# Kernel tuning notes

Hardware: AMD Instinct MI355X
Metric: run time of the kernel (lower is better)

The kernel has to match this reference:

```python
import jax, jax.numpy as jnp
import numpy as np

N, E, D, H, G, L = 50000, 800000, 64, 2, 512, 3  # nodes, edges, hidden, heads, graphs, layers


def setup_inputs() -> dict:
    key = jax.random.key(0)
    ks = jax.random.split(key, 20)
    x = jax.random.normal(ks[0], (N, D), dtype=jnp.float32)
    edge_index = jax.random.randint(ks[1], (2, E), 0, N, dtype=jnp.int64)
    batch = jnp.sort(jax.random.randint(ks[2], (N,), 0, G, dtype=jnp.int64))
    s = 1.0 / np.sqrt(D)
    Wq = jax.random.normal(ks[3], (L, D, H * D), dtype=jnp.float32) * s
    bq = jnp.zeros((L, H * D), jnp.float32)
    Wk = jax.random.normal(ks[4], (L, D, H * D), dtype=jnp.float32) * s
    bk = jnp.zeros((L, H * D), jnp.float32)
    Wv = jax.random.normal(ks[5], (L, D, H * D), dtype=jnp.float32) * s
    bv = jnp.zeros((L, H * D), jnp.float32)
    Ws = jax.random.normal(ks[6], (L, D, D), dtype=jnp.float32) * s
    bs = jnp.zeros((L, D), jnp.float32)
    ln_g = jnp.ones((L - 1, D), jnp.float32)
    ln_b = jnp.zeros((L - 1, D), jnp.float32)
    Wout = jax.random.normal(ks[7], (D, 1), dtype=jnp.float32) * s
    bout = jnp.zeros((1,), jnp.float32)
    return {"x": x, "edge_index": edge_index, "batch": batch, "num_graphs": G,
            "Wq": Wq, "bq": bq, "Wk": Wk, "bk": bk, "Wv": Wv, "bv": bv,
            "Ws": Ws, "bs": bs, "ln_g": ln_g, "ln_b": ln_b, "Wout": Wout, "bout": bout}


def _transformer_conv(x, src, dst, Wq, bq, Wk, bk, Wv, bv, Ws, bs):
    n = x.shape[0]
    q = (x @ Wq + bq).reshape(n, H, D)
    k = (x @ Wk + bk).reshape(n, H, D)
    v = (x @ Wv + bv).reshape(n, H, D)
    # per-edge attention score: q_dst . k_src / sqrt(d)
    scores = jnp.einsum('ehc,ehc->eh', q[dst], k[src]) / jnp.sqrt(jnp.float32(D))
    m = jax.ops.segment_max(scores, dst, num_segments=n)          # [n,H]
    e = jnp.exp(scores - m[dst])
    denom = jax.ops.segment_sum(e, dst, num_segments=n)           # [n,H]
    alpha = e / (denom[dst] + 1e-16)
    msg = alpha[..., None] * v[src]                               # [E,H,D]
    out = jax.ops.segment_sum(msg, dst, num_segments=n)           # [n,H,D]
    return out.mean(axis=1) + x @ Ws + bs                         # concat=False: head mean + skip


def _layernorm(x, g, b):
    mu = x.mean(-1, keepdims=True)
    var = ((x - mu) ** 2).mean(-1, keepdims=True)
    return (x - mu) / jnp.sqrt(var + 1e-5) * g + b


def reference(x, edge_index, batch, num_graphs, Wq, bq, Wk, bk, Wv, bv, Ws, bs, ln_g, ln_b, Wout, bout):
    src, dst = edge_index[0], edge_index[1]
    h = x
    for i in range(L):
        h = _transformer_conv(h, src, dst, Wq[i], bq[i], Wk[i], bk[i], Wv[i], bv[i], Ws[i], bs[i])
        h = jax.nn.relu(h)
        if i != L - 1:
            h = _layernorm(h, ln_g[i], ln_b[i])
    # global mean pool over graphs
    sums = jax.ops.segment_sum(h, batch, num_segments=num_graphs)
    cnt = jax.ops.segment_sum(jnp.ones((h.shape[0],), h.dtype), batch, num_segments=num_graphs)
    pooled = sums / jnp.maximum(cnt, 1.0)[:, None]
    return pooled @ Wout + bout
```

## Files before the change

### kernel.cpp

```cpp
#include <hip/hip_runtime.h>
#include <hip/hip_fp16.h>
#include <math.h>

#define NN 50000
#define EE 800000
#define GG 512

typedef _Float16 f16x8 __attribute__((ext_vector_type(8)));
typedef _Float16 f16x2 __attribute__((ext_vector_type(2)));
typedef float f32x4 __attribute__((ext_vector_type(4)));

#if defined(__has_builtin)
#if __has_builtin(__builtin_amdgcn_fdot2)
#define HAS_FDOT2 1
#endif
#endif

#define QSCALE 0.1803368801111244f

__device__ __forceinline__ float wave16_sum(float p) {
    p += __shfl_xor(p, 1);
    p += __shfl_xor(p, 2);
    p += __shfl_xor(p, 4);
    p += __shfl_xor(p, 8);
    return p;
}
__device__ __forceinline__ float2 h2f(unsigned int u) {
    __half2 h = *reinterpret_cast<__half2*>(&u);
    return __half22float2(h);
}
__device__ __forceinline__ unsigned short f2us(float x) {
    return __half_as_ushort(__float2half(x));
}
__device__ __forceinline__ float us2f(unsigned short u) {
    return __half2float(__ushort_as_half(u));
}
__device__ __forceinline__ f16x2 u2h2(unsigned int u) {
    union { unsigned int u; f16x2 h; } x; x.u = u; return x.h;
}
__device__ __forceinline__ float dot2acc(f16x2 a, f16x2 b, float c) {
#ifdef HAS_FDOT2
    return __builtin_amdgcn_fdot2(a, b, c, false);
#else
    return c + (float)a[0] * (float)b[0] + (float)a[1] * (float)b[1];
#endif
}
__device__ __forceinline__ float exp2fast(float x) {
    return __builtin_amdgcn_exp2f(x);
}

__global__ void deg_kernel(const int* __restrict__ ei, int* __restrict__ deg) {
    int e = blockIdx.x * 256 + threadIdx.x;
    if (e < EE) atomicAdd(&deg[ei[EE + e]], 1);
}

__global__ void scan1(const int* __restrict__ deg, int* __restrict__ incl, int* __restrict__ bsum) {
    __shared__ int sh[256];
    int t = threadIdx.x;
    int n = blockIdx.x * 256 + t;
    int vv = (n < NN) ? deg[n] : 0;
    sh[t] = vv; __syncthreads();
    for (int off = 1; off < 256; off <<= 1) {
        int u = (t >= off) ? sh[t - off] : 0;
        __syncthreads();
        sh[t] += u;
        __syncthreads();
    }
    if (n < NN) incl[n] = sh[t];
    if (t == 255) bsum[blockIdx.x] = sh[255];
}

__global__ void scan2(int* __restrict__ bsum, int nblk) {
    __shared__ int sh[256];
    int t = threadIdx.x;
    int vv = (t < nblk) ? bsum[t] : 0;
    sh[t] = vv; __syncthreads();
    for (int off = 1; off < 256; off <<= 1) {
        int u = (t >= off) ? sh[t - off] : 0;
        __syncthreads();
        sh[t] += u;
        __syncthreads();
    }
    bsum[t] = sh[t];
}

__global__ void scan3(int* __restrict__ rowst, const int* __restrict__ deg,
                      const int* __restrict__ bsum, int* __restrict__ cursor) {
    int n = blockIdx.x * 256 + threadIdx.x;
    if (n >= NN) return;
    int off = (blockIdx.x > 0) ? bsum[blockIdx.x - 1] : 0;
    int excl = rowst[n] - deg[n] + off;
    rowst[n] = excl;
    cursor[n] = excl;
}

__global__ void fill_kernel(const int* __restrict__ ei, int* __restrict__ cursor,
                            unsigned short* __restrict__ esrc) {
    int e = blockIdx.x * 256 + threadIdx.x;
    if (e < EE) {
        int s = ei[e], d = ei[EE + e];
        int pos = atomicAdd(&cursor[d], 1);
        esrc[pos] = (unsigned short)s;
    }
}

__global__ void cast_x_kernel(const float* __restrict__ x, unsigned short* __restrict__ xh) {
    int i = blockIdx.x * 256 + threadIdx.x;
    if (i < NN * 16) {
        float4 v = *(const float4*)(x + (size_t)i * 4);
        ushort4 o = make_ushort4(f2us(v.x), f2us(v.y), f2us(v.z), f2us(v.w));
        *(ushort4*)(xh + (size_t)i * 4) = o;
    }
}

#define WT_LSTRIDE (448 * 64)
__global__ void pack_w_kernel(const float* __restrict__ Wq, const float* __restrict__ Wk,
                              const float* __restrict__ Wv, const float* __restrict__ Ws,
                              unsigned short* __restrict__ wt) {
    int idx = blockIdx.x * 256 + threadIdx.x;
    if (idx >= 3 * WT_LSTRIDE) return;
    int l = idx / WT_LSTRIDE, r = idx % WT_LSTRIDE;
    int c = r / 64, k = r % 64;
    float val;
    if (c < 384) {
        int m = c >> 7, col = c & 127;
        const float* W = (m == 0) ? Wq : ((m == 1) ? Wk : Wv);
        val = W[(size_t)l * 64 * 128 + k * 128 + col];
    } else {
        int col = c - 384;
        val = Ws[(size_t)l * 64 * 64 + k * 64 + col];
    }
    wt[idx] = f2us(val);
}

__global__ __launch_bounds__(256) void gemm_mfma(
    const unsigned short* __restrict__ xh,
    const unsigned short* __restrict__ wt,
    const float* __restrict__ bq, const float* __restrict__ bk,
    const float* __restrict__ bv, const float* __restrict__ bsk,
    unsigned short* __restrict__ qh, unsigned short* __restrict__ kvh,
    float* __restrict__ skip) {
    int t = threadIdx.x;
    int wave = t >> 6, lane = t & 63;
    int li = lane & 15, lh = lane >> 4;
    int row0 = blockIdx.x * 32 + (wave & 1) * 16;
    int ctbase = (wave >> 1) * 14;

    int arow = min(row0 + li, NN - 1);
    const unsigned short* ap = xh + (size_t)arow * 64 + lh * 8;
    f16x8 a0 = *(const f16x8*)(ap);
    f16x8 a1 = *(const f16x8*)(ap + 32);

    int rb = row0 + lh * 4;

    #pragma unroll 2
    for (int tt = 0; tt < 14; ++tt) {
        int c = (ctbase + tt) * 16 + li;
        const unsigned short* bp = wt + (size_t)c * 64 + lh * 8;
        f16x8 b0 = *(const f16x8*)(bp);
        f16x8 b1 = *(const f16x8*)(bp + 32);
        f32x4 d = {0.f, 0.f, 0.f, 0.f};
        d = __builtin_amdgcn_mfma_f32_16x16x32_f16(a0, b0, d, 0, 0, 0);
        d = __builtin_amdgcn_mfma_f32_16x16x32_f16(a1, b1, d, 0, 0, 0);
        if (c < 128) {
            float bias = bq[c];
            #pragma unroll
            for (int e = 0; e < 4; ++e) {
                int r = rb + e;
                if (r < NN) qh[(size_t)r * 128 + c] = f2us((d[e] + bias) * QSCALE);
            }
        } else if (c < 256) {
            int ch = c - 128;
            float bias = bk[ch];
            int off = (ch < 64) ? ((ch >> 2) * 16 + (ch & 3))
                                : (((ch - 64) >> 2) * 16 + 4 + (ch & 3));
            #pragma unroll
            for (int e = 0; e < 4; ++e) {
                int r = rb + e;
                if (r < NN) kvh[(size_t)r * 256 + off] = f2us(d[e] + bias);
            }
        } else if (c < 384) {
            int ch = c - 256;
            float bias = bv[ch];
            int off = 8 + ((ch < 64) ? ((ch >> 2) * 16 + (ch & 3))
                                     : (((ch - 64) >> 2) * 16 + 4 + (ch & 3)));
            #pragma unroll
            for (int e = 0; e < 4; ++e) {
                int r = rb + e;
                if (r < NN) kvh[(size_t)r * 256 + off] = f2us(d[e] + bias);
            }
        } else {
            int ch = c - 384;
            float bias = bsk[ch];
            #pragma unroll
            for (int e = 0; e < 4; ++e) {
                int r = rb + e;
                if (r < NN) skip[(size_t)r * 64 + ch] = d[e] + bias;
            }
        }
    }
}

__global__ __launch_bounds__(256) void agg_kernel(
    const unsigned short* __restrict__ qh, const unsigned short* __restrict__ kvh,
    const float* __restrict__ skip,
    const int* __restrict__ rowst, const int* __restrict__ deg,
    const unsigned short* __restrict__ esrc, const float* __restrict__ gamma,
    const float* __restrict__ beta, unsigned short* __restrict__ hout, int do_ln) {
    int wave = threadIdx.x >> 6;
    int lane = threadIdx.x & 63;
    int node = blockIdx.x * 4 + wave;
    if (node >= NN) return;
    int j = lane & 15;
    int slot = lane >> 4;

    uint2 qu0 = *(const uint2*)(qh + (size_t)node * 128 + j * 4);
    uint2 qu1 = *(const uint2*)(qh + (size_t)node * 128 + 64 + j * 4);
    f16x2 q0a = u2h2(qu0.x), q0b = u2h2(qu0.y);
    f16x2 q1a = u2h2(qu1.x), q1b = u2h2(qu1.y);

    float m0 = -1e30f, m1 = -1e30f;
    float l0 = 0.f, l1 = 0.f;
    float acc0[4] = {0.f, 0.f, 0.f, 0.f};
    float acc1[4] = {0.f, 0.f, 0.f, 0.f};

    int st = rowst[node];
    int dg = deg[node];
    for (int base = slot * 2; base < dg; base += 8) {
        int last = dg - 1;
        int s0 = (int)esrc[st + min(base + 0, last)];
        int s1 = (int)esrc[st + min(base + 1, last)];
        const unsigned short* b0 = kvh + (size_t)s0 * 256 + j * 16;
        const unsigned short* b1 = kvh + (size_t)s1 * 256 + j * 16;
        uint4 A0 = *(const uint4*)(b0);
        uint4 B0 = *(const uint4*)(b0 + 8);
        uint4 A1 = *(const uint4*)(b1);
        uint4 B1 = *(const uint4*)(b1 + 8);

        float p00 = dot2acc(q0b, u2h2(A0.y), dot2acc(q0a, u2h2(A0.x), 0.f));
        float p01 = dot2acc(q1b, u2h2(A0.w), dot2acc(q1a, u2h2(A0.z), 0.f));
        float p10 = dot2acc(q0b, u2h2(A1.y), dot2acc(q0a, u2h2(A1.x), 0.f));
        float p11 = dot2acc(q1b, u2h2(A1.w), dot2acc(q1a, u2h2(A1.z), 0.f));
        p00 = wave16_sum(p00);
        p01 = wave16_sum(p01);
        p10 = wave16_sum(p10);
        p11 = wave16_sum(p11);
        if (base + 1 > last) { p10 = -1e30f; p11 = -1e30f; }

        float2 c00 = h2f(B0.x), c01 = h2f(B0.y), c02 = h2f(B0.z), c03 = h2f(B0.w);
        float2 c10 = h2f(B1.x), c11 = h2f(B1.y), c12 = h2f(B1.z), c13 = h2f(B1.w);
        float v00[4] = {c00.x, c00.y, c01.x, c01.y};
        float v01[4] = {c02.x, c02.y, c03.x, c03.y};
        float v10[4] = {c10.x, c10.y, c11.x, c11.y};
        float v11[4] = {c12.x, c12.y, c13.x, c13.y};

        {
            float nm = fmaxf(m0, fmaxf(p00, p10));
            float f = exp2fast(m0 - nm);
            float e0 = exp2fast(p00 - nm);
            float e1 = exp2fast(p10 - nm);
            l0 = l0 * f + e0 + e1;
            #pragma unroll
            for (int r = 0; r < 4; ++r)
                acc0[r] = acc0[r] * f + e0 * v00[r] + e1 * v10[r];
            m0 = nm;
        }
        {
            float nm = fmaxf(m1, fmaxf(p01, p11));
            float f = exp2fast(m1 - nm);
            float e0 = exp2fast(p01 - nm);
            float e1 = exp2fast(p11 - nm);
            l1 = l1 * f + e0 + e1;
            #pragma unroll
            for (int r = 0; r < 4; ++r)
                acc1[r] = acc1[r] * f + e0 * v01[r] + e1 * v11[r];
            m1 = nm;
        }
    }
    #pragma unroll
    for (int mask = 16; mask <= 32; mask <<= 1) {
        {
            float mo = __shfl_xor(m0, mask);
            float lo = __shfl_xor(l0, mask);
            float ao[4];
            #pragma unroll
            for (int r = 0; r < 4; ++r) ao[r] = __shfl_xor(acc0[r], mask);
            float nm = fmaxf(m0, mo);
            float fa = exp2fast(m0 - nm);
            float fb = exp2fast(mo - nm);
            l0 = l0 * fa + lo * fb;
            #pragma unroll
            for (int r = 0; r < 4; ++r) acc0[r] = acc0[r] * fa + ao[r] * fb;
            m0 = nm;
        }
        {
            float mo = __shfl_xor(m1, mask);
            float lo = __shfl_xor(l1, mask);
            float ao[4];
            #pragma unroll
            for (int r = 0; r < 4; ++r) ao[r] = __shfl_xor(acc1[r], mask);
            float nm = fmaxf(m1, mo);
            float fa = exp2fast(m1 - nm);
            float fb = exp2fast(mo - nm);
            l1 = l1 * fa + lo * fb;
            #pragma unroll
            for (int r = 0; r < 4; ++r) acc1[r] = acc1[r] * fa + ao[r] * fb;
            m1 = nm;
        }
    }
    float i0 = 1.f / (l0 + 1e-16f);
    float i1 = 1.f / (l1 + 1e-16f);
    float4 sk = *(const float4*)(skip + (size_t)node * 64 + j * 4);
    float ska[4] = {sk.x, sk.y, sk.z, sk.w};
    float val[4];
    #pragma unroll
    for (int r = 0; r < 4; ++r) {
        float o = 0.5f * (acc0[r] * i0 + acc1[r] * i1) + ska[r];
        val[r] = fmaxf(o, 0.f);
    }
    if (do_ln) {
        float s = val[0] + val[1] + val[2] + val[3];
        s = wave16_sum(s);
        float mu = s * (1.f / 64.f);
        float ss = 0.f;
        #pragma unroll
        for (int r = 0; r < 4; ++r) { float d = val[r] - mu; ss += d * d; }
        ss = wave16_sum(ss);
        float rstd = rsqrtf(ss * (1.f / 64.f) + 1e-5f);
        float4 g4 = *(const float4*)(gamma + j * 4);
        float4 b4 = *(const float4*)(beta + j * 4);
        float ga[4] = {g4.x, g4.y, g4.z, g4.w};
        float ba[4] = {b4.x, b4.y, b4.z, b4.w};
        #pragma unroll
        for (int r = 0; r < 4; ++r) val[r] = (val[r] - mu) * rstd * ga[r] + ba[r];
    }
    if (slot == 0) {
        ushort4 o = make_ushort4(f2us(val[0]), f2us(val[1]), f2us(val[2]), f2us(val[3]));
        *(ushort4*)(hout + (size_t)node * 64 + j * 4) = o;
    }
}

__device__ __forceinline__ int lbound(const int* __restrict__ a, int n, int key) {
    int lo = 0, hi = n;
    while (lo < hi) {
        int mid = (lo + hi) >> 1;
        if (a[mid] < key) lo = mid + 1; else hi = mid;
    }
    return lo;
}

__global__ __launch_bounds__(256) void pool_final_kernel(
    const unsigned short* __restrict__ h, const int* __restrict__ batch,
    const float* __restrict__ Wout, const float* __restrict__ bout,
    float* __restrict__ out) {
    __shared__ int sh_lo, sh_hi;
    __shared__ float part[4][64];
    int g = blockIdx.x;
    int t = threadIdx.x;
    if (t == 0) {
        sh_lo = lbound(batch, NN, g);
        sh_hi = lbound(batch, NN, g + 1);
    }
    __syncthreads();
    int lo = sh_lo, hi = sh_hi;
    int c = t & 63, w = t >> 6;
    float s = 0.f;
    for (int n = lo + w; n < hi; n += 4) s += us2f(h[(size_t)n * 64 + c]);
    part[w][c] = s;
    __syncthreads();
    if (t < 64) {
        float tot = part[0][t] + part[1][t] + part[2][t] + part[3][t];
        float cnt = (float)(hi - lo);
        float val = tot / fmaxf(cnt, 1.f) * Wout[t];
        #pragma unroll
        for (int mk = 1; mk < 64; mk <<= 1) val += __shfl_xor(val, mk);
        if (t == 0) out[g] = val + bout[0];
    }
}

extern "C" void kernel_launch(void* const* d_in, const int* in_sizes, int n_in,
                              void* d_out, int out_size, void* d_ws, size_t ws_size,
                              hipStream_t stream) {
    const float* x    = (const float*)d_in[0];
    const int*   ei   = (const int*)d_in[1];
    const int*   batch= (const int*)d_in[2];
    const float* Wq   = (const float*)d_in[4];
    const float* bq   = (const float*)d_in[5];
    const float* Wk   = (const float*)d_in[6];
    const float* bk   = (const float*)d_in[7];
    const float* Wv   = (const float*)d_in[8];
    const float* bv   = (const float*)d_in[9];
    const float* Ws   = (const float*)d_in[10];
    const float* bs   = (const float*)d_in[11];
    const float* lng  = (const float*)d_in[12];
    const float* lnb  = (const float*)d_in[13];
    const float* Wout = (const float*)d_in[14];
    const float* bout = (const float*)d_in[15];
    float* out = (float*)d_out;

    unsigned short* qh  = (unsigned short*)d_ws;
    unsigned short* kvh = qh + (size_t)NN * 128;
    float* skip = (float*)(kvh + (size_t)NN * 256);
    unsigned short* xh0 = (unsigned short*)(skip + (size_t)NN * 64);
    unsigned short* xh1 = xh0 + (size_t)NN * 64;
    unsigned short* wt  = xh1 + (size_t)NN * 64;
    int* deg    = (int*)(wt + 3 * WT_LSTRIDE);
    int* rowst  = deg + NN;
    int* cursor = rowst + NN;
    int* bsum   = cursor + NN;
    unsigned short* esrc = (unsigned short*)(bsum + 256);

    hipMemsetAsync(deg, 0, NN * sizeof(int), stream);

    const int NB = (NN + 255) / 256;
    deg_kernel<<<(EE + 255) / 256, 256, 0, stream>>>(ei, deg);
    scan1<<<NB, 256, 0, stream>>>(deg, rowst, bsum);
    scan2<<<1, 256, 0, stream>>>(bsum, NB);
    scan3<<<NB, 256, 0, stream>>>(rowst, deg, bsum, cursor);
    fill_kernel<<<(EE + 255) / 256, 256, 0, stream>>>(ei, cursor, esrc);

    cast_x_kernel<<<(NN * 16 + 255) / 256, 256, 0, stream>>>(x, xh0);
    pack_w_kernel<<<(3 * WT_LSTRIDE + 255) / 256, 256, 0, stream>>>(Wq, Wk, Wv, Ws, wt);

    const int GEMM_GRID = (NN + 31) / 32;
    unsigned short* hin = xh0;
    unsigned short* houts[3] = {xh1, xh0, xh1};
    for (int l = 0; l < 3; ++l) {
        gemm_mfma<<<GEMM_GRID, 256, 0, stream>>>(hin, wt + (size_t)l * WT_LSTRIDE,
            bq + (size_t)l * 128, bk + (size_t)l * 128, bv + (size_t)l * 128,
            bs + (size_t)l * 64, qh, kvh, skip);
        int do_ln = (l < 2) ? 1 : 0;
        agg_kernel<<<(NN + 3) / 4, 256, 0, stream>>>(qh, kvh, skip, rowst, deg, esrc,
                                                     lng + (size_t)(do_ln ? l : 0) * 64,
                                                     lnb + (size_t)(do_ln ? l : 0) * 64,
                                                     houts[l], do_ln);
        hin = houts[l];
    }
    pool_final_kernel<<<GG, 256, 0, stream>>>(hin, batch, Wout, bout, out);
}
```

Before: 404.7 us.

## Process two nodes per wave in aggregation with prefetched edge indices; fuse prep kernels

```diff
diff --git a/kernel.cpp b/kernel.cpp
--- a/kernel.cpp
+++ b/kernel.cpp
@@ -104,20 +104,19 @@
     }
 }
 
-__global__ void cast_x_kernel(const float* __restrict__ x, unsigned short* __restrict__ xh) {
+#define WT_LSTRIDE (448 * 64)
+__global__ void prep_kernel(const float* __restrict__ x, unsigned short* __restrict__ xh,
+                            const float* __restrict__ Wq, const float* __restrict__ Wk,
+                            const float* __restrict__ Wv, const float* __restrict__ Ws,
+                            unsigned short* __restrict__ wt) {
     int i = blockIdx.x * 256 + threadIdx.x;
     if (i < NN * 16) {
         float4 v = *(const float4*)(x + (size_t)i * 4);
         ushort4 o = make_ushort4(f2us(v.x), f2us(v.y), f2us(v.z), f2us(v.w));
         *(ushort4*)(xh + (size_t)i * 4) = o;
-    }
-}
-
-#define WT_LSTRIDE (448 * 64)
-__global__ void pack_w_kernel(const float* __restrict__ Wq, const float* __restrict__ Wk,
-                              const float* __restrict__ Wv, const float* __restrict__ Ws,
-                              unsigned short* __restrict__ wt) {
-    int idx = blockIdx.x * 256 + threadIdx.x;
+        return;
+    }
+    int idx = i - NN * 16;
     if (idx >= 3 * WT_LSTRIDE) return;
     int l = idx / WT_LSTRIDE, r = idx % WT_LSTRIDE;
     int c = r / 64, k = r % 64;
@@ -209,134 +208,270 @@
     const float* __restrict__ beta, unsigned short* __restrict__ hout, int do_ln) {
     int wave = threadIdx.x >> 6;
     int lane = threadIdx.x & 63;
-    int node = blockIdx.x * 4 + wave;
-    if (node >= NN) return;
+    int nodeA = blockIdx.x * 8 + wave * 2;
+    if (nodeA >= NN) return;
+    int nodeB = nodeA + 1;
+    bool hasB = nodeB < NN;
+    int nodeBc = hasB ? nodeB : nodeA;
     int j = lane & 15;
     int slot = lane >> 4;
 
-    uint2 qu0 = *(const uint2*)(qh + (size_t)node * 128 + j * 4);
-    uint2 qu1 = *(const uint2*)(qh + (size_t)node * 128 + 64 + j * 4);
-    f16x2 q0a = u2h2(qu0.x), q0b = u2h2(qu0.y);
-    f16x2 q1a = u2h2(qu1.x), q1b = u2h2(qu1.y);
-
-    float m0 = -1e30f, m1 = -1e30f;
-    float l0 = 0.f, l1 = 0.f;
-    float acc0[4] = {0.f, 0.f, 0.f, 0.f};
-    float acc1[4] = {0.f, 0.f, 0.f, 0.f};
-
-    int st = rowst[node];
-    int dg = deg[node];
-    for (int base = slot * 2; base < dg; base += 8) {
-        int last = dg - 1;
-        int s0 = (int)esrc[st + min(base + 0, last)];
-        int s1 = (int)esrc[st + min(base + 1, last)];
-        const unsigned short* b0 = kvh + (size_t)s0 * 256 + j * 16;
-        const unsigned short* b1 = kvh + (size_t)s1 * 256 + j * 16;
-        uint4 A0 = *(const uint4*)(b0);
-        uint4 B0 = *(const uint4*)(b0 + 8);
-        uint4 A1 = *(const uint4*)(b1);
-        uint4 B1 = *(const uint4*)(b1 + 8);
-
-        float p00 = dot2acc(q0b, u2h2(A0.y), dot2acc(q0a, u2h2(A0.x), 0.f));
-        float p01 = dot2acc(q1b, u2h2(A0.w), dot2acc(q1a, u2h2(A0.z), 0.f));
-        float p10 = dot2acc(q0b, u2h2(A1.y), dot2acc(q0a, u2h2(A1.x), 0.f));
-        float p11 = dot2acc(q1b, u2h2(A1.w), dot2acc(q1a, u2h2(A1.z), 0.f));
-        p00 = wave16_sum(p00);
-        p01 = wave16_sum(p01);
-        p10 = wave16_sum(p10);
-        p11 = wave16_sum(p11);
-        if (base + 1 > last) { p10 = -1e30f; p11 = -1e30f; }
-
-        float2 c00 = h2f(B0.x), c01 = h2f(B0.y), c02 = h2f(B0.z), c03 = h2f(B0.w);
-        float2 c10 = h2f(B1.x), c11 = h2f(B1.y), c12 = h2f(B1.z), c13 = h2f(B1.w);
-        float v00[4] = {c00.x, c00.y, c01.x, c01.y};
-        float v01[4] = {c02.x, c02.y, c03.x, c03.y};
-        float v10[4] = {c10.x, c10.y, c11.x, c11.y};
-        float v11[4] = {c12.x, c12.y, c13.x, c13.y};
+    uint2 qAu0 = *(const uint2*)(qh + (size_t)nodeA * 128 + j * 4);
+    uint2 qAu1 = *(const uint2*)(qh + (size_t)nodeA * 128 + 64 + j * 4);
+    uint2 qBu0 = *(const uint2*)(qh + (size_t)nodeBc * 128 + j * 4);
+    uint2 qBu1 = *(const uint2*)(qh + (size_t)nodeBc * 128 + 64 + j * 4);
+    f16x2 qA0a = u2h2(qAu0.x), qA0b = u2h2(qAu0.y);
+    f16x2 qA1a = u2h2(qAu1.x), qA1b = u2h2(qAu1.y);
+    f16x2 qB0a = u2h2(qBu0.x), qB0b = u2h2(qBu0.y);
+    f16x2 qB1a = u2h2(qBu1.x), qB1b = u2h2(qBu1.y);
+
+    float mA0 = -1e30f, mA1 = -1e30f, lA0 = 0.f, lA1 = 0.f;
+    float mB0 = -1e30f, mB1 = -1e30f, lB0 = 0.f, lB1 = 0.f;
+    float accA0[4] = {0.f, 0.f, 0.f, 0.f};
+    float accA1[4] = {0.f, 0.f, 0.f, 0.f};
+    float accB0[4] = {0.f, 0.f, 0.f, 0.f};
+    float accB1[4] = {0.f, 0.f, 0.f, 0.f};
+
+    int stA = rowst[nodeA], dgA = deg[nodeA];
+    int stB = rowst[nodeBc], dgB = hasB ? deg[nodeBc] : 0;
+    int lastA = max(dgA - 1, 0), lastB = max(dgB - 1, 0);
+    int dgMax = max(dgA, dgB);
+    int iters = (dgMax + 7) >> 3;
+    int b0 = slot * 2;
+
+    int sA0 = (dgA > 0) ? (int)esrc[stA + min(b0, lastA)] : 0;
+    int sA1 = (dgA > 0) ? (int)esrc[stA + min(b0 + 1, lastA)] : 0;
+    int sB0 = (dgB > 0) ? (int)esrc[stB + min(b0, lastB)] : 0;
+    int sB1 = (dgB > 0) ? (int)esrc[stB + min(b0 + 1, lastB)] : 0;
+
+    for (int it = 0; it < iters; ++it) {
+        int base = it * 8 + b0;
+        const unsigned short* a0p = kvh + (size_t)sA0 * 256 + j * 16;
+        const unsigned short* a1p = kvh + (size_t)sA1 * 256 + j * 16;
+        const unsigned short* b0p = kvh + (size_t)sB0 * 256 + j * 16;
+        const unsigned short* b1p = kvh + (size_t)sB1 * 256 + j * 16;
+        uint4 KA0 = *(const uint4*)(a0p);
+        uint4 VA0 = *(const uint4*)(a0p + 8);
+        uint4 KA1 = *(const uint4*)(a1p);
+        uint4 VA1 = *(const uint4*)(a1p + 8);
+        uint4 KB0 = *(const uint4*)(b0p);
+        uint4 VB0 = *(const uint4*)(b0p + 8);
+        uint4 KB1 = *(const uint4*)(b1p);
+        uint4 VB1 = *(const uint4*)(b1p + 8);
+
+        int nb = base + 8;
+        sA0 = (dgA > 0) ? (int)esrc[stA + min(nb, lastA)] : 0;
+        sA1 = (dgA > 0) ? (int)esrc[stA + min(nb + 1, lastA)] : 0;
+        sB0 = (dgB > 0) ? (int)esrc[stB + min(nb, lastB)] : 0;
+        sB1 = (dgB > 0) ? (int)esrc[stB + min(nb + 1, lastB)] : 0;
 
         {
-            float nm = fmaxf(m0, fmaxf(p00, p10));
-            float f = exp2fast(m0 - nm);
-            float e0 = exp2fast(p00 - nm);
-            float e1 = exp2fast(p10 - nm);
-            l0 = l0 * f + e0 + e1;
-            #pragma unroll
-            for (int r = 0; r < 4; ++r)
-                acc0[r] = acc0[r] * f + e0 * v00[r] + e1 * v10[r];
-            m0 = nm;
+            float p00 = dot2acc(qA0b, u2h2(KA0.y), dot2acc(qA0a, u2h2(KA0.x), 0.f));
+            float p01 = dot2acc(qA1b, u2h2(KA0.w), dot2acc(qA1a, u2h2(KA0.z), 0.f));
+            float p10 = dot2acc(qA0b, u2h2(KA1.y), dot2acc(qA0a, u2h2(KA1.x), 0.f));
+            float p11 = dot2acc(qA1b, u2h2(KA1.w), dot2acc(qA1a, u2h2(KA1.z), 0.f));
+            p00 = wave16_sum(p00);
+            p01 = wave16_sum(p01);
+            p10 = wave16_sum(p10);
+            p11 = wave16_sum(p11);
+            if (base > lastA || dgA == 0) { p00 = -1e30f; p01 = -1e30f; }
+            if (base + 1 > lastA || dgA == 0) { p10 = -1e30f; p11 = -1e30f; }
+
+            float2 c00 = h2f(VA0.x), c01 = h2f(VA0.y), c02 = h2f(VA0.z), c03 = h2f(VA0.w);
+            float2 c10 = h2f(VA1.x), c11 = h2f(VA1.y), c12 = h2f(VA1.z), c13 = h2f(VA1.w);
+            float v00[4] = {c00.x, c00.y, c01.x, c01.y};
+            float v01[4] = {c02.x, c02.y, c03.x, c03.y};
+            float v10[4] = {c10.x, c10.y, c11.x, c11.y};
+            float v11[4] = {c12.x, c12.y, c13.x, c13.y};
+            {
+                float nm = fmaxf(mA0, fmaxf(p00, p10));
+                float f = exp2fast(mA0 - nm);
+                float e0 = exp2fast(p00 - nm);
+                float e1 = exp2fast(p10 - nm);
+                lA0 = lA0 * f + e0 + e1;
+                #pragma unroll
+                for (int r = 0; r < 4; ++r)
+                    accA0[r] = accA0[r] * f + e0 * v00[r] + e1 * v10[r];
+                mA0 = nm;
+            }
+            {
+                float nm = fmaxf(mA1, fmaxf(p01, p11));
+                float f = exp2fast(mA1 - nm);
+                float e0 = exp2fast(p01 - nm);
+                float e1 = exp2fast(p11 - nm);
+                lA1 = lA1 * f + e0 + e1;
+                #pragma unroll
+                for (int r = 0; r < 4; ++r)
+                    accA1[r] = accA1[r] * f + e0 * v01[r] + e1 * v11[r];
+                mA1 = nm;
+            }
         }
         {
-            float nm = fmaxf(m1, fmaxf(p01, p11));
-            float f = exp2fast(m1 - nm);
-            float e0 = exp2fast(p01 - nm);
-            float e1 = exp2fast(p11 - nm);
-            l1 = l1 * f + e0 + e1;
-            #pragma unroll
-            for (int r = 0; r < 4; ++r)
-                acc1[r] = acc1[r] * f + e0 * v01[r] + e1 * v11[r];
-            m1 = nm;
-        }
-    }
+            float p00 = dot2acc(qB0b, u2h2(KB0.y), dot2acc(qB0a, u2h2(KB0.x), 0.f));
+            float p01 = dot2acc(qB1b, u2h2(KB0.w), dot2acc(qB1a, u2h2(KB0.z), 0.f));
+            float p10 = dot2acc(qB0b, u2h2(KB1.y), dot2acc(qB0a, u2h2(KB1.x), 0.f));
+            float p11 = dot2acc(qB1b, u2h2(KB1.w), dot2acc(qB1a, u2h2(KB1.z), 0.f));
+            p00 = wave16_sum(p00);
+            p01 = wave16_sum(p01);
+            p10 = wave16_sum(p10);
+            p11 = wave16_sum(p11);
+            if (base > lastB || dgB == 0) { p00 = -1e30f; p01 = -1e30f; }
+            if (base + 1 > lastB || dgB == 0) { p10 = -1e30f; p11 = -1e30f; }
+
+            float2 c00 = h2f(VB0.x), c01 = h2f(VB0.y), c02 = h2f(VB0.z), c03 = h2f(VB0.w);
+            float2 c10 = h2f(VB1.x), c11 = h2f(VB1.y), c12 = h2f(VB1.z), c13 = h2f(VB1.w);
+            float v00[4] = {c00.x, c00.y, c01.x, c01.y};
+            float v01[4] = {c02.x, c02.y, c03.x, c03.y};
+            float v10[4] = {c10.x, c10.y, c11.x, c11.y};
+            float v11[4] = {c12.x, c12.y, c13.x, c13.y};
+            {
+                float nm = fmaxf(mB0, fmaxf(p00, p10));
+                float f = exp2fast(mB0 - nm);
+                float e0 = exp2fast(p00 - nm);
+                float e1 = exp2fast(p10 - nm);
+                lB0 = lB0 * f + e0 + e1;
+                #pragma unroll
+                for (int r = 0; r < 4; ++r)
+                    accB0[r] = accB0[r] * f + e0 * v00[r] + e1 * v10[r];
+                mB0 = nm;
+            }
+            {
+                float nm = fmaxf(mB1, fmaxf(p01, p11));
+                float f = exp2fast(mB1 - nm);
+                float e0 = exp2fast(p01 - nm);
+                float e1 = exp2fast(p11 - nm);
+                lB1 = lB1 * f + e0 + e1;
+                #pragma unroll
+                for (int r = 0; r < 4; ++r)
+                    accB1[r] = accB1[r] * f + e0 * v01[r] + e1 * v11[r];
+                mB1 = nm;
+            }
+        }
+    }
+
     #pragma unroll
     for (int mask = 16; mask <= 32; mask <<= 1) {
         {
-            float mo = __shfl_xor(m0, mask);
-            float lo = __shfl_xor(l0, mask);
+            float mo = __shfl_xor(mA0, mask);
+            float lo = __shfl_xor(lA0, mask);
             float ao[4];
             #pragma unroll
-            for (int r = 0; r < 4; ++r) ao[r] = __shfl_xor(acc0[r], mask);
-            float nm = fmaxf(m0, mo);
-            float fa = exp2fast(m0 - nm);
+            for (int r = 0; r < 4; ++r) ao[r] = __shfl_xor(accA0[r], mask);
+            float nm = fmaxf(mA0, mo);
+            float fa = exp2fast(mA0 - nm);
             float fb = exp2fast(mo - nm);
-            l0 = l0 * fa + lo * fb;
-            #pragma unroll
-            for (int r = 0; r < 4; ++r) acc0[r] = acc0[r] * fa + ao[r] * fb;
-            m0 = nm;
+            lA0 = lA0 * fa + lo * fb;
+            #pragma unroll
+            for (int r = 0; r < 4; ++r) accA0[r] = accA0[r] * fa + ao[r] * fb;
+            mA0 = nm;
         }
         {
-            float mo = __shfl_xor(m1, mask);
-            float lo = __shfl_xor(l1, mask);
+            float mo = __shfl_xor(mA1, mask);
+            float lo = __shfl_xor(lA1, mask);
             float ao[4];
             #pragma unroll
-            for (int r = 0; r < 4; ++r) ao[r] = __shfl_xor(acc1[r], mask);
-            float nm = fmaxf(m1, mo);
-            float fa = exp2fast(m1 - nm);
+            for (int r = 0; r < 4; ++r) ao[r] = __shfl_xor(accA1[r], mask);
+            float nm = fmaxf(mA1, mo);
+            float fa = exp2fast(mA1 - nm);
             float fb = exp2fast(mo - nm);
-            l1 = l1 * fa + lo * fb;
-            #pragma unroll
-            for (int r = 0; r < 4; ++r) acc1[r] = acc1[r] * fa + ao[r] * fb;
-            m1 = nm;
-        }
-    }
-    float i0 = 1.f / (l0 + 1e-16f);
-    float i1 = 1.f / (l1 + 1e-16f);
-    float4 sk = *(const float4*)(skip + (size_t)node * 64 + j * 4);
-    float ska[4] = {sk.x, sk.y, sk.z, sk.w};
-    float val[4];
-    #pragma unroll
-    for (int r = 0; r < 4; ++r) {
-        float o = 0.5f * (acc0[r] * i0 + acc1[r] * i1) + ska[r];
-        val[r] = fmaxf(o, 0.f);
-    }
-    if (do_ln) {
-        float s = val[0] + val[1] + val[2] + val[3];
-        s = wave16_sum(s);
-        float mu = s * (1.f / 64.f);
-        float ss = 0.f;
+            lA1 = lA1 * fa + lo * fb;
+            #pragma unroll
+            for (int r = 0; r < 4; ++r) accA1[r] = accA1[r] * fa + ao[r] * fb;
+            mA1 = nm;
+        }
+        {
+            float mo = __shfl_xor(mB0, mask);
+            float lo = __shfl_xor(lB0, mask);
+            float ao[4];
+            #pragma unroll
+            for (int r = 0; r < 4; ++r) ao[r] = __shfl_xor(accB0[r], mask);
+            float nm = fmaxf(mB0, mo);
+            float fa = exp2fast(mB0 - nm);
+            float fb = exp2fast(mo - nm);
+            lB0 = lB0 * fa + lo * fb;
+            #pragma unroll
+            for (int r = 0; r < 4; ++r) accB0[r] = accB0[r] * fa + ao[r] * fb;
+            mB0 = nm;
+        }
+        {
+            float mo = __shfl_xor(mB1, mask);
+            float lo = __shfl_xor(lB1, mask);
+            float ao[4];
+            #pragma unroll
+            for (int r = 0; r < 4; ++r) ao[r] = __shfl_xor(accB1[r], mask);
+            float nm = fmaxf(mB1, mo);
+            float fa = exp2fast(mB1 - nm);
+            float fb = exp2fast(mo - nm);
+            lB1 = lB1 * fa + lo * fb;
+            #pragma unroll
+            for (int r = 0; r < 4; ++r) accB1[r] = accB1[r] * fa + ao[r] * fb;
+            mB1 = nm;
+        }
+    }
+
+    {
+        float i0 = 1.f / (lA0 + 1e-16f);
+        float i1 = 1.f / (lA1 + 1e-16f);
+        float4 sk = *(const float4*)(skip + (size_t)nodeA * 64 + j * 4);
+        float ska[4] = {sk.x, sk.y, sk.z, sk.w};
+        float val[4];
         #pragma unroll
-        for (int r = 0; r < 4; ++r) { float d = val[r] - mu; ss += d * d; }
-        ss = wave16_sum(ss);
-        float rstd = rsqrtf(ss * (1.f / 64.f) + 1e-5f);
-        float4 g4 = *(const float4*)(gamma + j * 4);
-        float4 b4 = *(const float4*)(beta + j * 4);
-        float ga[4] = {g4.x, g4.y, g4.z, g4.w};
-        float ba[4] = {b4.x, b4.y, b4.z, b4.w};
+        for (int r = 0; r < 4; ++r) {
+            float o = 0.5f * (accA0[r] * i0 + accA1[r] * i1) + ska[r];
+            val[r] = fmaxf(o, 0.f);
+        }
+        if (do_ln) {
+            float s = val[0] + val[1] + val[2] + val[3];
+            s = wave16_sum(s);
+            float mu = s * (1.f / 64.f);
+            float ss = 0.f;
+            #pragma unroll
+            for (int r = 0; r < 4; ++r) { float d = val[r] - mu; ss += d * d; }
+            ss = wave16_sum(ss);
+            float rstd = rsqrtf(ss * (1.f / 64.f) + 1e-5f);
+            float4 g4 = *(const float4*)(gamma + j * 4);
+            float4 b4 = *(const float4*)(beta + j * 4);
+            float ga[4] = {g4.x, g4.y, g4.z, g4.w};
+            float ba[4] = {b4.x, b4.y, b4.z, b4.w};
+            #pragma unroll
+            for (int r = 0; r < 4; ++r) val[r] = (val[r] - mu) * rstd * ga[r] + ba[r];
+        }
+        if (slot == 0) {
+            ushort4 o = make_ushort4(f2us(val[0]), f2us(val[1]), f2us(val[2]), f2us(val[3]));
+            *(ushort4*)(hout + (size_t)nodeA * 64 + j * 4) = o;
+        }
+    }
+    if (hasB) {
+        float i0 = 1.f / (lB0 + 1e-16f);
+        float i1 = 1.f / (lB1 + 1e-16f);
+        float4 sk = *(const float4*)(skip + (size_t)nodeB * 64 + j * 4);
+        float ska[4] = {sk.x, sk.y, sk.z, sk.w};
+        float val[4];
         #pragma unroll
-        for (int r = 0; r < 4; ++r) val[r] = (val[r] - mu) * rstd * ga[r] + ba[r];
-    }
-    if (slot == 0) {
-        ushort4 o = make_ushort4(f2us(val[0]), f2us(val[1]), f2us(val[2]), f2us(val[3]));
-        *(ushort4*)(hout + (size_t)node * 64 + j * 4) = o;
+        for (int r = 0; r < 4; ++r) {
+            float o = 0.5f * (accB0[r] * i0 + accB1[r] * i1) + ska[r];
+            val[r] = fmaxf(o, 0.f);
+        }
+        if (do_ln) {
+            float s = val[0] + val[1] + val[2] + val[3];
+            s = wave16_sum(s);
+            float mu = s * (1.f / 64.f);
+            float ss = 0.f;
+            #pragma unroll
+            for (int r = 0; r < 4; ++r) { float d = val[r] - mu; ss += d * d; }
+            ss = wave16_sum(ss);
+            float rstd = rsqrtf(ss * (1.f / 64.f) + 1e-5f);
+            float4 g4 = *(const float4*)(gamma + j * 4);
+            float4 b4 = *(const float4*)(beta + j * 4);
+            float ga[4] = {g4.x, g4.y, g4.z, g4.w};
+            float ba[4] = {b4.x, b4.y, b4.z, b4.w};
+            #pragma unroll
+            for (int r = 0; r < 4; ++r) val[r] = (val[r] - mu) * rstd * ga[r] + ba[r];
+        }
+        if (slot == 0) {
+            ushort4 o = make_ushort4(f2us(val[0]), f2us(val[1]), f2us(val[2]), f2us(val[3]));
+            *(ushort4*)(hout + (size_t)nodeB * 64 + j * 4) = o;
+        }
     }
 }
 
@@ -419,8 +554,8 @@
     scan3<<<NB, 256, 0, stream>>>(rowst, deg, bsum, cursor);
     fill_kernel<<<(EE + 255) / 256, 256, 0, stream>>>(ei, cursor, esrc);
 
-    cast_x_kernel<<<(NN * 16 + 255) / 256, 256, 0, stream>>>(x, xh0);
-    pack_w_kernel<<<(3 * WT_LSTRIDE + 255) / 256, 256, 0, stream>>>(Wq, Wk, Wv, Ws, wt);
+    const int PREP_TOT = NN * 16 + 3 * WT_LSTRIDE;
+    prep_kernel<<<(PREP_TOT + 255) / 256, 256, 0, stream>>>(x, xh0, Wq, Wk, Wv, Ws, wt);
 
     const int GEMM_GRID = (NN + 31) / 32;
     unsigned short* hin = xh0;
@@ -430,7 +565,7 @@
             bq + (size_t)l * 128, bk + (size_t)l * 128, bv + (size_t)l * 128,
             bs + (size_t)l * 64, qh, kvh, skip);
         int do_ln = (l < 2) ? 1 : 0;
-        agg_kernel<<<(NN + 3) / 4, 256, 0, stream>>>(qh, kvh, skip, rowst, deg, esrc,
+        agg_kernel<<<(NN + 7) / 8, 256, 0, stream>>>(qh, kvh, skip, rowst, deg, esrc,
                                                      lng + (size_t)(do_ln ? l : 0) * 64,
                                                      lnb + (size_t)(do_ln ? l : 0) * 64,
                                                      houts[l], do_ln);
```

Result: slower. 461.5 us (+14.0%).

## Store K and V contiguously per node and fuse input cast with weight packing

Applied to the files above, without the earlier changes.

```diff
diff --git a/kernel.cpp b/kernel.cpp
--- a/kernel.cpp
+++ b/kernel.cpp
@@ -104,20 +104,19 @@
     }
 }
 
-__global__ void cast_x_kernel(const float* __restrict__ x, unsigned short* __restrict__ xh) {
+#define WT_LSTRIDE (448 * 64)
+__global__ void prep_kernel(const float* __restrict__ x, unsigned short* __restrict__ xh,
+                            const float* __restrict__ Wq, const float* __restrict__ Wk,
+                            const float* __restrict__ Wv, const float* __restrict__ Ws,
+                            unsigned short* __restrict__ wt) {
     int i = blockIdx.x * 256 + threadIdx.x;
     if (i < NN * 16) {
         float4 v = *(const float4*)(x + (size_t)i * 4);
         ushort4 o = make_ushort4(f2us(v.x), f2us(v.y), f2us(v.z), f2us(v.w));
         *(ushort4*)(xh + (size_t)i * 4) = o;
-    }
-}
-
-#define WT_LSTRIDE (448 * 64)
-__global__ void pack_w_kernel(const float* __restrict__ Wq, const float* __restrict__ Wk,
-                              const float* __restrict__ Wv, const float* __restrict__ Ws,
-                              unsigned short* __restrict__ wt) {
-    int idx = blockIdx.x * 256 + threadIdx.x;
+        return;
+    }
+    int idx = i - NN * 16;
     if (idx >= 3 * WT_LSTRIDE) return;
     int l = idx / WT_LSTRIDE, r = idx % WT_LSTRIDE;
     int c = r / 64, k = r % 64;
@@ -172,22 +171,18 @@
         } else if (c < 256) {
             int ch = c - 128;
             float bias = bk[ch];
-            int off = (ch < 64) ? ((ch >> 2) * 16 + (ch & 3))
-                                : (((ch - 64) >> 2) * 16 + 4 + (ch & 3));
             #pragma unroll
             for (int e = 0; e < 4; ++e) {
                 int r = rb + e;
-                if (r < NN) kvh[(size_t)r * 256 + off] = f2us(d[e] + bias);
+                if (r < NN) kvh[(size_t)r * 256 + ch] = f2us(d[e] + bias);
             }
         } else if (c < 384) {
             int ch = c - 256;
             float bias = bv[ch];
-            int off = 8 + ((ch < 64) ? ((ch >> 2) * 16 + (ch & 3))
-                                     : (((ch - 64) >> 2) * 16 + 4 + (ch & 3)));
             #pragma unroll
             for (int e = 0; e < 4; ++e) {
                 int r = rb + e;
-                if (r < NN) kvh[(size_t)r * 256 + off] = f2us(d[e] + bias);
+                if (r < NN) kvh[(size_t)r * 256 + 128 + ch] = f2us(d[e] + bias);
             }
         } else {
             int ch = c - 384;
@@ -226,29 +221,35 @@
 
     int st = rowst[node];
     int dg = deg[node];
+    int last = dg - 1;
     for (int base = slot * 2; base < dg; base += 8) {
-        int last = dg - 1;
         int s0 = (int)esrc[st + min(base + 0, last)];
         int s1 = (int)esrc[st + min(base + 1, last)];
-        const unsigned short* b0 = kvh + (size_t)s0 * 256 + j * 16;
-        const unsigned short* b1 = kvh + (size_t)s1 * 256 + j * 16;
-        uint4 A0 = *(const uint4*)(b0);
-        uint4 B0 = *(const uint4*)(b0 + 8);
-        uint4 A1 = *(const uint4*)(b1);
-        uint4 B1 = *(const uint4*)(b1 + 8);
-
-        float p00 = dot2acc(q0b, u2h2(A0.y), dot2acc(q0a, u2h2(A0.x), 0.f));
-        float p01 = dot2acc(q1b, u2h2(A0.w), dot2acc(q1a, u2h2(A0.z), 0.f));
-        float p10 = dot2acc(q0b, u2h2(A1.y), dot2acc(q0a, u2h2(A1.x), 0.f));
-        float p11 = dot2acc(q1b, u2h2(A1.w), dot2acc(q1a, u2h2(A1.z), 0.f));
+        const unsigned short* b0 = kvh + (size_t)s0 * 256;
+        const unsigned short* b1 = kvh + (size_t)s1 * 256;
+        uint2 K00 = *(const uint2*)(b0 + j * 4);
+        uint2 K01 = *(const uint2*)(b0 + 64 + j * 4);
+        uint2 V00 = *(const uint2*)(b0 + 128 + j * 4);
+        uint2 V01 = *(const uint2*)(b0 + 192 + j * 4);
+        uint2 K10 = *(const uint2*)(b1 + j * 4);
+        uint2 K11 = *(const uint2*)(b1 + 64 + j * 4);
+        uint2 V10 = *(const uint2*)(b1 + 128 + j * 4);
+        uint2 V11 = *(const uint2*)(b1 + 192 + j * 4);
+
+        float p00 = dot2acc(q0b, u2h2(K00.y), dot2acc(q0a, u2h2(K00.x), 0.f));
+        float p01 = dot2acc(q1b, u2h2(K01.y), dot2acc(q1a, u2h2(K01.x), 0.f));
+        float p10 = dot2acc(q0b, u2h2(K10.y), dot2acc(q0a, u2h2(K10.x), 0.f));
+        float p11 = dot2acc(q1b, u2h2(K11.y), dot2acc(q1a, u2h2(K11.x), 0.f));
         p00 = wave16_sum(p00);
         p01 = wave16_sum(p01);
         p10 = wave16_sum(p10);
         p11 = wave16_sum(p11);
         if (base + 1 > last) { p10 = -1e30f; p11 = -1e30f; }
 
-        float2 c00 = h2f(B0.x), c01 = h2f(B0.y), c02 = h2f(B0.z), c03 = h2f(B0.w);
-        float2 c10 = h2f(B1.x), c11 = h2f(B1.y), c12 = h2f(B1.z), c13 = h2f(B1.w);
+        float2 c00 = h2f(V00.x), c01 = h2f(V00.y);
+        float2 c02 = h2f(V01.x), c03 = h2f(V01.y);
+        float2 c10 = h2f(V10.x), c11 = h2f(V10.y);
+        float2 c12 = h2f(V11.x), c13 = h2f(V11.y);
         float v00[4] = {c00.x, c00.y, c01.x, c01.y};
         float v01[4] = {c02.x, c02.y, c03.x, c03.y};
         float v10[4] = {c10.x, c10.y, c11.x, c11.y};
@@ -419,8 +420,8 @@
     scan3<<<NB, 256, 0, stream>>>(rowst, deg, bsum, cursor);
     fill_kernel<<<(EE + 255) / 256, 256, 0, stream>>>(ei, cursor, esrc);
 
-    cast_x_kernel<<<(NN * 16 + 255) / 256, 256, 0, stream>>>(x, xh0);
-    pack_w_kernel<<<(3 * WT_LSTRIDE + 255) / 256, 256, 0, stream>>>(Wq, Wk, Wv, Ws, wt);
+    const int PREP_TOT = NN * 16 + 3 * WT_LSTRIDE;
+    prep_kernel<<<(PREP_TOT + 255) / 256, 256, 0, stream>>>(x, xh0, Wq, Wk, Wv, Ws, wt);
 
     const int GEMM_GRID = (NN + 31) / 32;
     unsigned short* hin = xh0;
```

Result: faster. 395.4 us (-2.3%).

## Stage GEMM outputs in LDS for coalesced stores, fp16 skip, fuse prep kernels

Applied to the files above, without the earlier changes.

```diff
diff --git a/kernel.cpp b/kernel.cpp
--- a/kernel.cpp
+++ b/kernel.cpp
@@ -104,33 +104,46 @@
     }
 }
 
-__global__ void cast_x_kernel(const float* __restrict__ x, unsigned short* __restrict__ xh) {
-    int i = blockIdx.x * 256 + threadIdx.x;
-    if (i < NN * 16) {
+#define WT_LSTRIDE (448 * 64)
+#define XCAST_BLKS 3125
+__global__ void prep_kernel(const float* __restrict__ x, unsigned short* __restrict__ xh,
+                            const float* __restrict__ Wq, const float* __restrict__ Wk,
+                            const float* __restrict__ Wv, const float* __restrict__ Ws,
+                            unsigned short* __restrict__ wt) {
+    __shared__ float lds_t[64][65];
+    if (blockIdx.x < XCAST_BLKS) {
+        int i = blockIdx.x * 256 + threadIdx.x;
         float4 v = *(const float4*)(x + (size_t)i * 4);
         ushort4 o = make_ushort4(f2us(v.x), f2us(v.y), f2us(v.z), f2us(v.w));
         *(ushort4*)(xh + (size_t)i * 4) = o;
-    }
-}
-
-#define WT_LSTRIDE (448 * 64)
-__global__ void pack_w_kernel(const float* __restrict__ Wq, const float* __restrict__ Wk,
-                              const float* __restrict__ Wv, const float* __restrict__ Ws,
-                              unsigned short* __restrict__ wt) {
-    int idx = blockIdx.x * 256 + threadIdx.x;
-    if (idx >= 3 * WT_LSTRIDE) return;
-    int l = idx / WT_LSTRIDE, r = idx % WT_LSTRIDE;
-    int c = r / 64, k = r % 64;
-    float val;
-    if (c < 384) {
-        int m = c >> 7, col = c & 127;
-        const float* W = (m == 0) ? Wq : ((m == 1) ? Wk : Wv);
-        val = W[(size_t)l * 64 * 128 + k * 128 + col];
-    } else {
-        int col = c - 384;
-        val = Ws[(size_t)l * 64 * 64 + k * 64 + col];
-    }
-    wt[idx] = f2us(val);
+        return;
+    }
+    int tile = blockIdx.x - XCAST_BLKS;
+    int l = tile / 7, ct = tile % 7;
+    int c0 = ct * 64;
+    int t = threadIdx.x;
+    #pragma unroll
+    for (int r = 0; r < 16; ++r) {
+        int idx = r * 256 + t;
+        int kk = idx >> 6, cc = idx & 63;
+        int c = c0 + cc;
+        float val;
+        if (c < 384) {
+            int m = c >> 7, col = c & 127;
+            const float* W = (m == 0) ? Wq : ((m == 1) ? Wk : Wv);
+            val = W[(size_t)l * 8192 + kk * 128 + col];
+        } else {
+            val = Ws[(size_t)l * 4096 + kk * 64 + (c - 384)];
+        }
+        lds_t[cc][kk] = val;
+    }
+    __syncthreads();
+    #pragma unroll
+    for (int r = 0; r < 16; ++r) {
+        int idx = r * 256 + t;
+        int cc = idx >> 6, kk = idx & 63;
+        wt[((size_t)l * 448 + c0 + cc) * 64 + kk] = f2us(lds_t[cc][kk]);
+    }
 }
 
 __global__ __launch_bounds__(256) void gemm_mfma(
@@ -139,11 +152,15 @@
     const float* __restrict__ bq, const float* __restrict__ bk,
     const float* __restrict__ bv, const float* __restrict__ bsk,
     unsigned short* __restrict__ qh, unsigned short* __restrict__ kvh,
-    float* __restrict__ skip) {
+    unsigned short* __restrict__ skiph) {
+    __shared__ __align__(16) unsigned short lds_q[32 * 128];
+    __shared__ __align__(16) unsigned short lds_kv[32 * 256];
+    __shared__ __align__(16) unsigned short lds_sk[32 * 64];
     int t = threadIdx.x;
     int wave = t >> 6, lane = t & 63;
     int li = lane & 15, lh = lane >> 4;
-    int row0 = blockIdx.x * 32 + (wave & 1) * 16;
+    int brow = blockIdx.x * 32;
+    int row0 = brow + (wave & 1) * 16;
     int ctbase = (wave >> 1) * 14;
 
     int arow = min(row0 + li, NN - 1);
@@ -151,7 +168,7 @@
     f16x8 a0 = *(const f16x8*)(ap);
     f16x8 a1 = *(const f16x8*)(ap + 32);
 
-    int rb = row0 + lh * 4;
+    int rl0 = (wave & 1) * 16 + lh * 4;
 
     #pragma unroll 2
     for (int tt = 0; tt < 14; ++tt) {
@@ -165,45 +182,56 @@
         if (c < 128) {
             float bias = bq[c];
             #pragma unroll
-            for (int e = 0; e < 4; ++e) {
-                int r = rb + e;
-                if (r < NN) qh[(size_t)r * 128 + c] = f2us((d[e] + bias) * QSCALE);
-            }
+            for (int e = 0; e < 4; ++e)
+                lds_q[(rl0 + e) * 128 + c] = f2us((d[e] + bias) * QSCALE);
         } else if (c < 256) {
             int ch = c - 128;
             float bias = bk[ch];
             int off = (ch < 64) ? ((ch >> 2) * 16 + (ch & 3))
                                 : (((ch - 64) >> 2) * 16 + 4 + (ch & 3));
             #pragma unroll
-            for (int e = 0; e < 4; ++e) {
-                int r = rb + e;
-                if (r < NN) kvh[(size_t)r * 256 + off] = f2us(d[e] + bias);
-            }
+            for (int e = 0; e < 4; ++e)
+                lds_kv[(rl0 + e) * 256 + off] = f2us(d[e] + bias);
         } else if (c < 384) {
             int ch = c - 256;
             float bias = bv[ch];
             int off = 8 + ((ch < 64) ? ((ch >> 2) * 16 + (ch & 3))
                                      : (((ch - 64) >> 2) * 16 + 4 + (ch & 3)));
             #pragma unroll
-            for (int e = 0; e < 4; ++e) {
-                int r = rb + e;
-                if (r < NN) kvh[(size_t)r * 256 + off] = f2us(d[e] + bias);
-            }
+            for (int e = 0; e < 4; ++e)
+                lds_kv[(rl0 + e) * 256 + off] = f2us(d[e] + bias);
         } else {
             int ch = c - 384;
             float bias = bsk[ch];
             #pragma unroll
-            for (int e = 0; e < 4; ++e) {
-                int r = rb + e;
-                if (r < NN) skip[(size_t)r * 64 + ch] = d[e] + bias;
-            }
-        }
+            for (int e = 0; e < 4; ++e)
+                lds_sk[(rl0 + e) * 64 + ch] = f2us(d[e] + bias);
+        }
+    }
+    __syncthreads();
+    #pragma unroll
+    for (int i = t; i < 512; i += 256) {
+        int r = i >> 4, gr = brow + r;
+        if (gr < NN)
+            *(uint4*)(qh + (size_t)gr * 128 + (i & 15) * 8) = ((const uint4*)lds_q)[i];
+    }
+    #pragma unroll
+    for (int i = t; i < 1024; i += 256) {
+        int r = i >> 5, gr = brow + r;
+        if (gr < NN)
+            *(uint4*)(kvh + (size_t)gr * 256 + (i & 31) * 8) = ((const uint4*)lds_kv)[i];
+    }
+    {
+        int i = t;
+        int r = i >> 3, gr = brow + r;
+        if (i < 256 && gr < NN)
+            *(uint4*)(skiph + (size_t)gr * 64 + (i & 7) * 8) = ((const uint4*)lds_sk)[i];
     }
 }
 
 __global__ __launch_bounds__(256) void agg_kernel(
     const unsigned short* __restrict__ qh, const unsigned short* __restrict__ kvh,
-    const float* __restrict__ skip,
+    const unsigned short* __restrict__ skiph,
     const int* __restrict__ rowst, const int* __restrict__ deg,
     const unsigned short* __restrict__ esrc, const float* __restrict__ gamma,
     const float* __restrict__ beta, unsigned short* __restrict__ hout, int do_ln) {
@@ -226,8 +254,8 @@
 
     int st = rowst[node];
     int dg = deg[node];
+    int last = dg - 1;
     for (int base = slot * 2; base < dg; base += 8) {
-        int last = dg - 1;
         int s0 = (int)esrc[st + min(base + 0, last)];
         int s1 = (int)esrc[st + min(base + 1, last)];
         const unsigned short* b0 = kvh + (size_t)s0 * 256 + j * 16;
@@ -310,8 +338,9 @@
     }
     float i0 = 1.f / (l0 + 1e-16f);
     float i1 = 1.f / (l1 + 1e-16f);
-    float4 sk = *(const float4*)(skip + (size_t)node * 64 + j * 4);
-    float ska[4] = {sk.x, sk.y, sk.z, sk.w};
+    uint2 sku = *(const uint2*)(skiph + (size_t)node * 64 + j * 4);
+    float2 s0f = h2f(sku.x), s1f = h2f(sku.y);
+    float ska[4] = {s0f.x, s0f.y, s1f.x, s1f.y};
     float val[4];
     #pragma unroll
     for (int r = 0; r < 4; ++r) {
@@ -400,11 +429,11 @@
 
     unsigned short* qh  = (unsigned short*)d_ws;
     unsigned short* kvh = qh + (size_t)NN * 128;
-    float* skip = (float*)(kvh + (size_t)NN * 256);
-    unsigned short* xh0 = (unsigned short*)(skip + (size_t)NN * 64);
+    unsigned short* skiph = kvh + (size_t)NN * 256;
+    unsigned short* xh0 = skiph + (size_t)NN * 64;
     unsigned short* xh1 = xh0 + (size_t)NN * 64;
     unsigned short* wt  = xh1 + (size_t)NN * 64;
-    int* deg    = (int*)(wt + 3 * WT_LSTRIDE);
+    int* deg    = (int*)(wt + 3 * WT_LSTRIDE + 64);
     int* rowst  = deg + NN;
     int* cursor = rowst + NN;
     int* bsum   = cursor + NN;
@@ -419,8 +448,7 @@
     scan3<<<NB, 256, 0, stream>>>(rowst, deg, bsum, cursor);
     fill_kernel<<<(EE + 255) / 256, 256, 0, stream>>>(ei, cursor, esrc);
 
-    cast_x_kernel<<<(NN * 16 + 255) / 256, 256, 0, stream>>>(x, xh0);
-    pack_w_kernel<<<(3 * WT_LSTRIDE + 255) / 256, 256, 0, stream>>>(Wq, Wk, Wv, Ws, wt);
+    prep_kernel<<<XCAST_BLKS + 21, 256, 0, stream>>>(x, xh0, Wq, Wk, Wv, Ws, wt);
 
     const int GEMM_GRID = (NN + 31) / 32;
     unsigned short* hin = xh0;
@@ -428,9 +456,9 @@
     for (int l = 0; l < 3; ++l) {
         gemm_mfma<<<GEMM_GRID, 256, 0, stream>>>(hin, wt + (size_t)l * WT_LSTRIDE,
             bq + (size_t)l * 128, bk + (size_t)l * 128, bv + (size_t)l * 128,
-            bs + (size_t)l * 64, qh, kvh, skip);
+            bs + (size_t)l * 64, qh, kvh, skiph);
         int do_ln = (l < 2) ? 1 : 0;
-        agg_kernel<<<(NN + 3) / 4, 256, 0, stream>>>(qh, kvh, skip, rowst, deg, esrc,
+        agg_kernel<<<(NN + 3) / 4, 256, 0, stream>>>(qh, kvh, skiph, rowst, deg, esrc,
                                                      lng + (size_t)(do_ln ? l : 0) * 64,
                                                      lnb + (size_t)(do_ln ? l : 0) * 64,
                                                      houts[l], do_ln);
```

After: 395.0 us. 2.4% less time.
